# Kernel optimization log

Measured on AMD Instinct MI355X. Metric: run time of the kernel, lower is better.

## Reference

```python
import jax, jax.numpy as jnp
import numpy as np

N, D, NF = 65536, 512, 32  # samples, flattened dim, n_transformations


def setup_inputs() -> dict:
    key = jax.random.key(0)
    k1, k2, k3, k4 = jax.random.split(key, 4)
    lim = float(np.sqrt(1.0 / D))  # reset_parameters uniform bound
    x = jax.random.normal(k1, (N, D), dtype=jnp.float32)
    u = jax.random.uniform(k2, (NF, D), dtype=jnp.float32, minval=-lim, maxval=lim)
    w = jax.random.uniform(k3, (NF, D), dtype=jnp.float32, minval=-lim, maxval=lim)
    b = jax.random.uniform(k4, (NF,), dtype=jnp.float32, minval=-lim, maxval=lim)
    return {"x": x, "u": u, "w": w, "b": b}


def reference(x, u, w, b):
    """Chain of NF planar flows (nn.Sequential of SinglePlanarFlow).
    Returns (transformed samples [N,D], summed log|det J| per sample [N])."""

    def step(xc, params):
        ui, wi, bi = params  # [D], [D], scalar
        wtu = jnp.dot(wi, ui)
        m_wtu = -1.0 + jnp.log1p(jnp.exp(wtu))
        # enforce invertibility: u_hat = u + (m(wtu)-wtu) * w / ||w||^2 when wtu < 1
        u_hat = jnp.where(wtu < 1.0, ui + (m_wtu - wtu) * wi / jnp.dot(wi, wi), ui)
        lin = xc @ wi + bi          # [N]
        t = jnp.tanh(lin)           # h(lin)
        out = xc + t[:, None] * u_hat
        # psi @ u_hat^T = h'(lin) * (w . u_hat)
        logdet = jnp.log(jnp.abs(1.0 + (1.0 - t * t) * jnp.dot(wi, u_hat)))  # [N]
        return out, logdet

    out, logdets = jax.lax.scan(step, x, (u, w, b))  # logdets: [NF, N]
    return out, jnp.sum(logdets, axis=0)
```

## Files before the change

### kernel.cpp

```cpp
#include <hip/hip_runtime.h>
#include <math.h>

#define NS 65536
#define DD 512
#define NF 32

__global__ __launch_bounds__(256) void k_uhat(const float* __restrict__ u,
                                              const float* __restrict__ w,
                                              float* __restrict__ u_hat) {
    const int i = blockIdx.x;
    const int tid = threadIdx.x;
    __shared__ float s_wu[256];
    __shared__ float s_ww[256];
    float pu = 0.f, pw = 0.f;
    for (int d = tid; d < DD; d += 256) {
        float wv = w[i * DD + d];
        pu += wv * u[i * DD + d];
        pw += wv * wv;
    }
    s_wu[tid] = pu;
    s_ww[tid] = pw;
    __syncthreads();
    for (int s = 128; s > 0; s >>= 1) {
        if (tid < s) {
            s_wu[tid] += s_wu[tid + s];
            s_ww[tid] += s_ww[tid + s];
        }
        __syncthreads();
    }
    const float wtu = s_wu[0];
    const float ww  = s_ww[0];
    float scale = 0.f;
    if (wtu < 1.f) {
        float m = -1.f + log1pf(expf(wtu));
        scale = (m - wtu) / ww;
    }
    for (int d = tid; d < DD; d += 256) {
        u_hat[i * DD + d] = u[i * DD + d] + scale * w[i * DD + d];
    }
}

__global__ __launch_bounds__(256) void k_gmat(const float* __restrict__ u_hat,
                                              const float* __restrict__ w,
                                              float* __restrict__ G) {
    const int tid = blockIdx.x * 256 + threadIdx.x;
    const int i = tid >> 5;
    const int j = tid & 31;
    const float* uh = u_hat + i * DD;
    const float* wj = w + j * DD;
    float s = 0.f;
    for (int d = 0; d < DD; ++d) s += uh[d] * wj[d];
    G[i * NF + j] = s;
}

__global__ __launch_bounds__(256) void k_flow(const float* __restrict__ x,
                                              const float* __restrict__ w,
                                              const float* __restrict__ b,
                                              const float* __restrict__ u_hat,
                                              const float* __restrict__ G,
                                              float* __restrict__ out,
                                              float* __restrict__ logdet) {
    const int r = blockIdx.x * 256 + threadIdx.x;
    const float* xr = x + (size_t)r * DD;

    float lin[NF];
#pragma unroll
    for (int j = 0; j < NF; ++j) lin[j] = b[j];

    for (int c = 0; c < DD; c += 16) {
        const float4 x0 = *(const float4*)(xr + c);
        const float4 x1 = *(const float4*)(xr + c + 4);
        const float4 x2 = *(const float4*)(xr + c + 8);
        const float4 x3 = *(const float4*)(xr + c + 12);
#pragma unroll
        for (int j = 0; j < NF; ++j) {
            const float* wj = w + j * DD + c;
            float acc;
            acc  = x0.x * wj[0]  + x0.y * wj[1]  + x0.z * wj[2]  + x0.w * wj[3];
            acc += x1.x * wj[4]  + x1.y * wj[5]  + x1.z * wj[6]  + x1.w * wj[7];
            acc += x2.x * wj[8]  + x2.y * wj[9]  + x2.z * wj[10] + x2.w * wj[11];
            acc += x3.x * wj[12] + x3.y * wj[13] + x3.z * wj[14] + x3.w * wj[15];
            lin[j] += acc;
        }
    }

    float ldet = 0.f;
#pragma unroll
    for (int j = 0; j < NF; ++j) {
        const float t = tanhf(lin[j]);
        const float det = 1.f + (1.f - t * t) * G[j * NF + j];
        ldet += logf(fabsf(det));
#pragma unroll
        for (int i = j + 1; i < NF; ++i) lin[i] += t * G[j * NF + i];
        lin[j] = t;
    }

    float* outr = out + (size_t)r * DD;
    for (int c = 0; c < DD; c += 8) {
        float4 a0 = *(const float4*)(xr + c);
        float4 a1 = *(const float4*)(xr + c + 4);
#pragma unroll
        for (int j = 0; j < NF; ++j) {
            const float* uj = u_hat + j * DD + c;
            const float t = lin[j];
            a0.x += t * uj[0]; a0.y += t * uj[1]; a0.z += t * uj[2]; a0.w += t * uj[3];
            a1.x += t * uj[4]; a1.y += t * uj[5]; a1.z += t * uj[6]; a1.w += t * uj[7];
        }
        *(float4*)(outr + c)     = a0;
        *(float4*)(outr + c + 4) = a1;
    }
    logdet[r] = ldet;
}

extern "C" void kernel_launch(void* const* d_in, const int* in_sizes, int n_in,
                              void* d_out, int out_size, void* d_ws, size_t ws_size,
                              hipStream_t stream) {
    const float* x = (const float*)d_in[0];
    const float* u = (const float*)d_in[1];
    const float* w = (const float*)d_in[2];
    const float* b = (const float*)d_in[3];

    float* out    = (float*)d_out;
    float* logdet = out + (size_t)NS * DD;

    float* u_hat = (float*)d_ws;
    float* G     = u_hat + NF * DD;

    k_uhat<<<NF, 256, 0, stream>>>(u, w, u_hat);
    k_gmat<<<(NF * NF) / 256, 256, 0, stream>>>(u_hat, w, G);
    k_flow<<<NS / 256, 256, 0, stream>>>(x, w, b, u_hat, G, out, logdet);
}
```

Before: 525.3 us.

## Split planar flow into coalesced projection, recurrence, and output kernels

Replaces the one-thread-per-row fused kernel with three kernels. The first computes all x·w projections using LDS-staged, swizzled, coalesced x tiles. The second runs the sequential tanh recurrence and logdet per row on a compact [N,32] buffer. The third applies the output update with u_hat held in registers and lane-contiguous column access. This targets the poorly coalesced per-thread row reads in the old kernel, at the cost of extra launches, an intermediate buffer round trip, and a dependence on workspace size (the old kernel remains as a fallback).

After: 487.3 us. 1.08x faster.

```diff
diff --git a/kernel.cpp b/kernel.cpp
--- a/kernel.cpp
+++ b/kernel.cpp
@@ -53,6 +53,113 @@
     G[i * NF + j] = s;
 }
 
+#define KC 64
+
+__global__ __launch_bounds__(256) void k_lin(const float* __restrict__ x,
+                                             const float* __restrict__ w,
+                                             float* __restrict__ LT) {
+    __shared__ float xs[64 * KC];
+    const int t  = threadIdx.x;
+    const int jg = __builtin_amdgcn_readfirstlane(t >> 6);
+    const int rl = t & 63;
+    const int r0 = blockIdx.x * 64;
+
+    float acc[8];
+#pragma unroll
+    for (int jj = 0; jj < 8; ++jj) acc[jj] = 0.f;
+
+    for (int kc = 0; kc < DD; kc += KC) {
+        __syncthreads();
+#pragma unroll
+        for (int i = 0; i < 4; ++i) {
+            const int f   = i * 256 + t;
+            const int row = f >> 4;
+            const int c4  = f & 15;
+            const float4 v = *(const float4*)(x + (size_t)(r0 + row) * DD + kc + c4 * 4);
+            const int byte = row * 256 + ((c4 * 16) ^ ((row & 7) << 4));
+            *(float4*)((char*)xs + byte) = v;
+        }
+        __syncthreads();
+#pragma unroll
+        for (int c4 = 0; c4 < 16; ++c4) {
+            const int byte = rl * 256 + ((c4 * 16) ^ ((rl & 7) << 4));
+            const float4 xv = *(const float4*)((const char*)xs + byte);
+#pragma unroll
+            for (int jj = 0; jj < 8; ++jj) {
+                const float* wp = w + (size_t)(jg * 8 + jj) * DD + kc + c4 * 4;
+                acc[jj] += xv.x * wp[0] + xv.y * wp[1] + xv.z * wp[2] + xv.w * wp[3];
+            }
+        }
+    }
+    float* lp = LT + (size_t)(r0 + rl) * NF + jg * 8;
+    *(float4*)(lp)     = make_float4(acc[0], acc[1], acc[2], acc[3]);
+    *(float4*)(lp + 4) = make_float4(acc[4], acc[5], acc[6], acc[7]);
+}
+
+__global__ __launch_bounds__(256) void k_rec(float* __restrict__ LT,
+                                             const float* __restrict__ b,
+                                             const float* __restrict__ G,
+                                             float* __restrict__ logdet) {
+    const int r = blockIdx.x * 256 + threadIdx.x;
+    float* lp = LT + (size_t)r * NF;
+
+    float lin[NF];
+#pragma unroll
+    for (int j = 0; j < NF; j += 4) {
+        float4 v = *(const float4*)(lp + j);
+        lin[j] = v.x + b[j]; lin[j+1] = v.y + b[j+1];
+        lin[j+2] = v.z + b[j+2]; lin[j+3] = v.w + b[j+3];
+    }
+
+    float ldet = 0.f;
+#pragma unroll
+    for (int j = 0; j < NF; ++j) {
+        const float tt = tanhf(lin[j]);
+        const float gd = G[j * NF + j];
+        ldet += logf(fabsf(1.f + (1.f - tt * tt) * gd));
+#pragma unroll
+        for (int i = j + 1; i < NF; ++i) lin[i] = fmaf(tt, G[j * NF + i], lin[i]);
+        lin[j] = tt;
+    }
+
+#pragma unroll
+    for (int j = 0; j < NF; j += 4) {
+        *(float4*)(lp + j) = make_float4(lin[j], lin[j+1], lin[j+2], lin[j+3]);
+    }
+    logdet[r] = ldet;
+}
+
+#define OUT_R 32
+
+__global__ __launch_bounds__(256) void k_out(const float* __restrict__ x,
+                                             const float* __restrict__ u_hat,
+                                             const float* __restrict__ T,
+                                             float* __restrict__ out) {
+    const int wid  = __builtin_amdgcn_readfirstlane(blockIdx.x * 4 + (threadIdx.x >> 6));
+    const int lane = threadIdx.x & 63;
+    const int cg   = wid & 1;
+    const int rg   = wid >> 1;
+    const int col  = cg * 256 + lane * 4;
+
+    float4 uh[NF];
+#pragma unroll
+    for (int j = 0; j < NF; ++j) uh[j] = *(const float4*)(u_hat + (size_t)j * DD + col);
+
+    for (int rr = 0; rr < OUT_R; ++rr) {
+        const int r = rg * OUT_R + rr;
+        float4 o = *(const float4*)(x + (size_t)r * DD + col);
+#pragma unroll
+        for (int j = 0; j < NF; ++j) {
+            const float tj = T[(size_t)r * NF + j];
+            o.x = fmaf(tj, uh[j].x, o.x);
+            o.y = fmaf(tj, uh[j].y, o.y);
+            o.z = fmaf(tj, uh[j].z, o.z);
+            o.w = fmaf(tj, uh[j].w, o.w);
+        }
+        *(float4*)(out + (size_t)r * DD + col) = o;
+    }
+}
+
 __global__ __launch_bounds__(256) void k_flow(const float* __restrict__ x,
                                               const float* __restrict__ w,
                                               const float* __restrict__ b,
@@ -62,11 +169,9 @@
                                               float* __restrict__ logdet) {
     const int r = blockIdx.x * 256 + threadIdx.x;
     const float* xr = x + (size_t)r * DD;
-
     float lin[NF];
 #pragma unroll
     for (int j = 0; j < NF; ++j) lin[j] = b[j];
-
     for (int c = 0; c < DD; c += 16) {
         const float4 x0 = *(const float4*)(xr + c);
         const float4 x1 = *(const float4*)(xr + c + 4);
@@ -83,7 +188,6 @@
             lin[j] += acc;
         }
     }
-
     float ldet = 0.f;
 #pragma unroll
     for (int j = 0; j < NF; ++j) {
@@ -94,7 +198,6 @@
         for (int i = j + 1; i < NF; ++i) lin[i] += t * G[j * NF + i];
         lin[j] = t;
     }
-
     float* outr = out + (size_t)r * DD;
     for (int c = 0; c < DD; c += 8) {
         float4 a0 = *(const float4*)(xr + c);
@@ -125,8 +228,18 @@
 
     float* u_hat = (float*)d_ws;
     float* G     = u_hat + NF * DD;
+    float* LT    = G + NF * NF;
+
+    const size_t need = (size_t)(NF * DD + NF * NF + (size_t)NS * NF) * sizeof(float);
 
     k_uhat<<<NF, 256, 0, stream>>>(u, w, u_hat);
     k_gmat<<<(NF * NF) / 256, 256, 0, stream>>>(u_hat, w, G);
-    k_flow<<<NS / 256, 256, 0, stream>>>(x, w, b, u_hat, G, out, logdet);
-}
+
+    if (ws_size >= need) {
+        k_lin<<<NS / 64, 256, 0, stream>>>(x, w, LT);
+        k_rec<<<NS / 256, 256, 0, stream>>>(LT, b, G, logdet);
+        k_out<<<(NS / OUT_R) * 2 / 4, 256, 0, stream>>>(x, u_hat, LT, out);
+    } else {
+        k_flow<<<NS / 256, 256, 0, stream>>>(x, w, b, u_hat, G, out, logdet);
+    }
+}
```
